# Kernel tuning notes

Hardware: AMD Instinct MI355X
Metric: run time of the kernel (lower is better)

## Reference

```python
import jax, jax.numpy as jnp
import numpy as np

N, E, B = 3000, 96000, 64
CIN, MID = 8, 16
G1, G2 = 32, 8
FC1, FC2, OUT = 512, 128, 10
EPS = 1e-5


def setup_inputs() -> dict:
    key = jax.random.key(0)
    ks = jax.random.split(key, 40)
    u = lambda k, shape, s: jax.random.uniform(k, shape, jnp.float32, -s, s)
    inp = {}
    inp['x'] = jax.random.normal(ks[0], (N, B, CIN), jnp.float32)
    inp['edge_index'] = jax.random.randint(ks[1], (2, E), 0, N, jnp.int64)
    # SAGEConv params (uniform(-1/sqrt(in_channels), ...))
    s = 1.0 / np.sqrt(CIN)
    inp['edge_w_raw'] = jnp.ones((E,), jnp.float32) * 0.01
    inp['sage_self_w'] = u(ks[2], (CIN, MID), s)
    inp['sage_w'] = u(ks[3], (CIN, MID), s)
    inp['sage_b'] = u(ks[4], (MID,), s)
    # LayerNorm over (num_nodes, mid_channel)
    inp['ln_g'] = jnp.ones((N, MID), jnp.float32)
    inp['ln_b'] = jnp.zeros((N, MID), jnp.float32)
    # 1x1 Conv2d stacks (stored as [out,in] matrices) + BatchNorm2d (eval stats)
    inp['conv1_w'] = jax.random.normal(ks[5], (G1, MID), jnp.float32) * np.sqrt(2.0 / G1)
    inp['conv1_b'] = u(ks[6], (G1,), 1.0 / np.sqrt(MID))
    inp['bn1_g'] = jax.random.uniform(ks[7], (G1,), jnp.float32, 0.5, 1.5)
    inp['bn1_b'] = jax.random.normal(ks[8], (G1,), jnp.float32) * 0.1
    inp['bn1_m'] = jax.random.normal(ks[9], (G1,), jnp.float32) * 0.1
    inp['bn1_v'] = jax.random.uniform(ks[10], (G1,), jnp.float32, 0.5, 1.5)
    inp['conv2_w'] = jax.random.normal(ks[11], (G2, G1), jnp.float32) * np.sqrt(2.0 / G2)
    inp['conv2_b'] = u(ks[12], (G2,), 1.0 / np.sqrt(G1))
    inp['bn2_g'] = jax.random.uniform(ks[13], (G2,), jnp.float32, 0.5, 1.5)
    inp['bn2_b'] = jax.random.normal(ks[14], (G2,), jnp.float32) * 0.1
    inp['bn2_m'] = jax.random.normal(ks[15], (G2,), jnp.float32) * 0.1
    inp['bn2_v'] = jax.random.uniform(ks[16], (G2,), jnp.float32, 0.5, 1.5)
    # FC stack: Linear(G2*N, FC1) + BN1d, Linear(FC1, FC2) + BN1d, fc1
    d0 = G2 * N
    inp['fc_w1'] = jax.random.normal(ks[17], (FC1, d0), jnp.float32) * np.sqrt(2.0 / (d0 + FC1))
    inp['fc_b1'] = jnp.full((FC1,), 0.01, jnp.float32)
    inp['bnf1_g'] = jax.random.uniform(ks[18], (FC1,), jnp.float32, 0.5, 1.5)
    inp['bnf1_b'] = jax.random.normal(ks[19], (FC1,), jnp.float32) * 0.1
    inp['bnf1_m'] = jax.random.normal(ks[20], (FC1,), jnp.float32) * 0.1
    inp['bnf1_v'] = jax.random.uniform(ks[21], (FC1,), jnp.float32, 0.5, 1.5)
    inp['fc_w2'] = jax.random.normal(ks[22], (FC2, FC1), jnp.float32) * np.sqrt(2.0 / (FC1 + FC2))
    inp['fc_b2'] = jnp.full((FC2,), 0.01, jnp.float32)
    inp['bnf2_g'] = jax.random.uniform(ks[23], (FC2,), jnp.float32, 0.5, 1.5)
    inp['bnf2_b'] = jax.random.normal(ks[24], (FC2,), jnp.float32) * 0.1
    inp['bnf2_m'] = jax.random.normal(ks[25], (FC2,), jnp.float32) * 0.1
    inp['bnf2_v'] = jax.random.uniform(ks[26], (FC2,), jnp.float32, 0.5, 1.5)
    inp['fc1_w'] = jax.random.normal(ks[27], (OUT, FC2), jnp.float32) * np.sqrt(2.0 / (FC2 + OUT))
    inp['fc1_b'] = jnp.full((OUT,), 0.01, jnp.float32)
    return inp


def _bn(y, g, b, m, v):
    # eval-mode BatchNorm; y is [B, C, N] or [B, C]
    if y.ndim == 3:
        return (y - m[:, None]) * (g[:, None] / jnp.sqrt(v[:, None] + EPS)) + b[:, None]
    return (y - m) * (g / jnp.sqrt(v + EPS)) + b


def reference(x, edge_index, edge_w_raw, sage_self_w, sage_w, sage_b, ln_g, ln_b,
              conv1_w, conv1_b, bn1_g, bn1_b, bn1_m, bn1_v,
              conv2_w, conv2_b, bn2_g, bn2_b, bn2_m, bn2_v,
              fc_w1, fc_b1, bnf1_g, bnf1_b, bnf1_m, bnf1_v,
              fc_w2, fc_b2, bnf2_g, bnf2_b, bnf2_m, bnf2_v,
              fc1_w, fc1_b):
    row, col = edge_index[0], edge_index[1]
    ew = jax.nn.sigmoid(edge_w_raw)
    # SAGEConv: gather -> weighted message -> scatter-mean by col -> matmul
    msg = x[row] * ew[:, None, None]                          # [E, B, CIN]
    summed = jax.ops.segment_sum(msg, col, num_segments=N)    # [N, B, CIN]
    cnt = jax.ops.segment_sum(jnp.ones((E,), x.dtype), col, num_segments=N)
    agg = summed / jnp.maximum(cnt, 1.0)[:, None, None]
    neigh = jnp.einsum('nbc,cm->nbm', agg, sage_w) + sage_b   # [N, B, MID]
    self_out = jnp.einsum('nbc,cm->nbm', x, sage_self_w)
    h = 0.0 * self_out + 1.0 * neigh                          # alphas = [0, 1]
    h = jax.nn.relu(h)
    # LayerNorm over (num_nodes, mid) per batch element
    hb = jnp.transpose(h, (1, 0, 2))                          # [B, N, MID]
    mu = hb.mean(axis=(1, 2), keepdims=True)
    var = hb.var(axis=(1, 2), keepdims=True)
    hb = (hb - mu) / jnp.sqrt(var + EPS) * ln_g + ln_b
    y = jnp.transpose(hb, (0, 2, 1))                          # [B, MID, N]
    # 1x1 conv stack (relu then BN, matching source order)
    y = jnp.einsum('om,bmn->bon', conv1_w, y) + conv1_b[:, None]
    y = _bn(jax.nn.relu(y), bn1_g, bn1_b, bn1_m, bn1_v)
    y = jnp.einsum('oc,bcn->bon', conv2_w, y) + conv2_b[:, None]
    y = _bn(jax.nn.relu(y), bn2_g, bn2_b, bn2_m, bn2_v)       # [B, G2, N]
    z = y.reshape(y.shape[0], -1)                             # [B, G2*N]
    z = jax.nn.relu(_bn(z @ fc_w1.T + fc_b1, bnf1_g, bnf1_b, bnf1_m, bnf1_v))
    z = jax.nn.relu(_bn(z @ fc_w2.T + fc_b2, bnf2_g, bnf2_b, bnf2_m, bnf2_v))
    logits = z @ fc1_w.T + fc1_b
    return jax.nn.softmax(logits, axis=-1), logits
```

## Files before the change

kernel.cpp:

```cpp
#include <hip/hip_runtime.h>
#include <hip/hip_bf16.h>
#include <math.h>

#define NN   3000
#define EE   96000
#define BB   64
#define CIN  8
#define MID  16
#define G1   32
#define G2   8
#define FC1N 512
#define FC2N 128
#define OUTN 10
#define EPSV 1e-5f

#define BC   (BB * CIN)
#define HROW (NN * MID)
#define D0   (G2 * NN)

#define P_EWRAW 0
#define P_SW    96000
#define P_SB    96128
#define P_LNG   96144
#define P_LNB   144144
#define P_C1W   192144
#define P_C1B   192656
#define P_BN1G  192688
#define P_BN1B  192720
#define P_BN1M  192752
#define P_BN1V  192784
#define P_C2W   192816
#define P_C2B   193072
#define P_BN2G  193080
#define P_BN2B  193088
#define P_BN2M  193096
#define P_BN2V  193104
#define P_FB1   193112
#define P_BF1G  193624
#define P_BF1B  194136
#define P_BF1M  194648
#define P_BF1V  195160
#define P_FW2   195672
#define P_FB2   261208
#define P_BF2G  261336
#define P_BF2B  261464
#define P_BF2M  261592
#define P_BF2V  261720
#define P_FOW   261848
#define P_FOB   263128
#define P_TOT   263138

#define KCH  320
#define NKC  75

__device__ __forceinline__ float b2f(unsigned short u) {
    union { unsigned int i; float f; } c;
    c.i = ((unsigned int)u) << 16;
    return c.f;
}

__device__ __forceinline__ unsigned short f2b_rne(float x) {
    union { float f; unsigned int u; } c; c.f = x;
    unsigned int r = c.u + 0x7FFFu + ((c.u >> 16) & 1u);
    return (unsigned short)(r >> 16);
}

typedef __attribute__((ext_vector_type(8))) short short8;
typedef __attribute__((ext_vector_type(4))) float f32x4;

struct PTab { const void* p[30]; };
__global__ __launch_bounds__(256)
void k_prep(const void* __restrict__ ei_raw, const unsigned int* __restrict__ ewr,
            PTab tab,
            int* __restrict__ ei32, int* __restrict__ cnt, int* __restrict__ flags,
            float* __restrict__ P) {
    __shared__ int sh_is64, sh_bf;
    if (threadIdx.x == 0) {
        const int* pw = (const int*)ei_raw;
        int any = 0;
        #pragma unroll
        for (int i = 1; i < 32; i += 2) any |= pw[i];
        sh_is64 = (any == 0) ? 1 : 0;
        unsigned int w = ewr[0];
        sh_bf = ((w >> 16) == (w & 0xFFFFu)) ? 1 : 0;
        if (blockIdx.x == 0) flags[0] = sh_bf;
    }
    __syncthreads();
    int bf = sh_bf;
    long long gi = (long long)blockIdx.x * blockDim.x + threadIdx.x;
    if (gi < 2 * EE) {
        int i = (int)gi;
        int v = sh_is64 ? (int)((const long long*)ei_raw)[i]
                        : ((const int*)ei_raw)[i];
        ei32[i] = v;
        if (i >= EE) atomicAdd(&cnt[v], 1);
        return;
    }
    gi -= 2 * EE;
    if (gi >= P_TOT) return;
    int i = (int)gi;
    const int off[31] = {
        P_EWRAW, P_SW, P_SB, P_LNG, P_LNB, P_C1W, P_C1B, P_BN1G, P_BN1B, P_BN1M,
        P_BN1V, P_C2W, P_C2B, P_BN2G, P_BN2B, P_BN2M, P_BN2V, P_FB1, P_BF1G,
        P_BF1B, P_BF1M, P_BF1V, P_FW2, P_FB2, P_BF2G, P_BF2B, P_BF2M, P_BF2V,
        P_FOW, P_FOB, P_TOT };
    int r = 0;
    #pragma unroll
    for (int j = 1; j < 31; ++j) r += (i >= off[j]) ? 1 : 0;
    int e = i - off[r];
    P[i] = bf ? b2f(((const unsigned short*)tab.p[r])[e])
              : ((const float*)tab.p[r])[e];
}

__global__ void k_scan(const int* __restrict__ cnt, int* __restrict__ off,
                       int* __restrict__ cursor) {
    __shared__ int part[1024];
    int t = threadIdx.x;
    int base = t * 3;
    int c0 = 0, c1 = 0, c2 = 0;
    if (base     < NN) c0 = cnt[base];
    if (base + 1 < NN) c1 = cnt[base + 1];
    if (base + 2 < NN) c2 = cnt[base + 2];
    int s = c0 + c1 + c2;
    part[t] = s;
    __syncthreads();
    for (int d = 1; d < 1024; d <<= 1) {
        int v = (t >= d) ? part[t - d] : 0;
        __syncthreads();
        part[t] += v;
        __syncthreads();
    }
    int excl = part[t] - s;
    if (base < NN)     { off[base]     = excl;           cursor[base]     = excl; }
    if (base + 1 < NN) { off[base + 1] = excl + c0;      cursor[base + 1] = excl + c0; }
    if (base + 2 < NN) { off[base + 2] = excl + c0 + c1; cursor[base + 2] = excl + c0 + c1; }
    if (t == 1023) off[NN] = part[1023];
}

__global__ void k_scatter(const int* __restrict__ ei, const float* __restrict__ ew,
                          int* __restrict__ cursor,
                          int* __restrict__ rcsr, float* __restrict__ wcsr) {
    int e = blockIdx.x * blockDim.x + threadIdx.x;
    if (e < EE) {
        int p = atomicAdd(&cursor[ei[EE + e]], 1);
        rcsr[p] = ei[e];
        wcsr[p] = 1.f / (1.f + expf(-ew[e]));
    }
}

__global__ __launch_bounds__(256)
void k_agg_sage(const void* __restrict__ xraw, const int* __restrict__ flags,
                const int* __restrict__ off,
                const int* __restrict__ rcsr, const float* __restrict__ wcsr,
                const float* __restrict__ sw, const float* __restrict__ sb,
                float* __restrict__ hb) {
    __shared__ float aggL[BC];
    __shared__ float swL[CIN * MID];
    __shared__ float sbL[MID];
    int n = blockIdx.x;
    int t = threadIdx.x;
    if (t < CIN * MID) swL[t] = sw[t];
    if (t < MID)       sbL[t] = sb[t];
    int k0 = off[n], k1 = off[n + 1];
    float a0 = 0.f, a1 = 0.f, b0 = 0.f, b1 = 0.f;
    int k = k0;
    if (flags[0]) {
        const unsigned int* xu = (const unsigned int*)xraw;
        for (; k + 3 < k1; k += 4) {
            int   r0 = rcsr[k],     r1 = rcsr[k + 1];
            int   r2 = rcsr[k + 2], r3 = rcsr[k + 3];
            float w0 = wcsr[k],     w1 = wcsr[k + 1];
            float w2 = wcsr[k + 2], w3 = wcsr[k + 3];
            unsigned int u0 = xu[(size_t)r0 * 256 + t];
            unsigned int u1 = xu[(size_t)r1 * 256 + t];
            unsigned int u2 = xu[(size_t)r2 * 256 + t];
            unsigned int u3 = xu[(size_t)r3 * 256 + t];
            a0 += b2f((unsigned short)(u0 & 0xFFFFu)) * w0;
            a1 += b2f((unsigned short)(u0 >> 16))     * w0;
            b0 += b2f((unsigned short)(u1 & 0xFFFFu)) * w1;
            b1 += b2f((unsigned short)(u1 >> 16))     * w1;
            a0 += b2f((unsigned short)(u2 & 0xFFFFu)) * w2;
            a1 += b2f((unsigned short)(u2 >> 16))     * w2;
            b0 += b2f((unsigned short)(u3 & 0xFFFFu)) * w3;
            b1 += b2f((unsigned short)(u3 >> 16))     * w3;
        }
        for (; k < k1; ++k) {
            int r0 = rcsr[k];
            float w0 = wcsr[k];
            unsigned int u0 = xu[(size_t)r0 * 256 + t];
            a0 += b2f((unsigned short)(u0 & 0xFFFFu)) * w0;
            a1 += b2f((unsigned short)(u0 >> 16))     * w0;
        }
        float inv = 1.f / fmaxf((float)(k1 - k0), 1.f);
        aggL[2 * t]     = (a0 + b0) * inv;
        aggL[2 * t + 1] = (a1 + b1) * inv;
    } else {
        const float* x = (const float*)xraw;
        for (; k + 3 < k1; k += 4) {
            int   r0 = rcsr[k],     r1 = rcsr[k + 1];
            int   r2 = rcsr[k + 2], r3 = rcsr[k + 3];
            float w0 = wcsr[k],     w1 = wcsr[k + 1];
            float w2 = wcsr[k + 2], w3 = wcsr[k + 3];
            const float* xp0 = x + (size_t)r0 * BC;
            const float* xp1 = x + (size_t)r1 * BC;
            const float* xp2 = x + (size_t)r2 * BC;
            const float* xp3 = x + (size_t)r3 * BC;
            a0 += xp0[t]       * w0;  a1 += xp0[t + 256] * w0;
            b0 += xp1[t]       * w1;  b1 += xp1[t + 256] * w1;
            a0 += xp2[t]       * w2;  a1 += xp2[t + 256] * w2;
            b0 += xp3[t]       * w3;  b1 += xp3[t + 256] * w3;
        }
        for (; k < k1; ++k) {
            int r0 = rcsr[k];
            float w0 = wcsr[k];
            const float* xp0 = x + (size_t)r0 * BC;
            a0 += xp0[t] * w0;
            a1 += xp0[t + 256] * w0;
        }
        float inv = 1.f / fmaxf((float)(k1 - k0), 1.f);
        aggL[t]       = (a0 + b0) * inv;
        aggL[t + 256] = (a1 + b1) * inv;
    }
    __syncthreads();
    #pragma unroll
    for (int r4 = 0; r4 < 4; ++r4) {
        int q = t + r4 * 256;
        int b = q >> 4, m = q & 15;
        float v = sbL[m];
        const float* ag = &aggL[b * CIN];
        #pragma unroll
        for (int c = 0; c < CIN; ++c) v += ag[c] * swL[c * MID + m];
        v = fmaxf(v, 0.f);
        hb[(size_t)b * HROW + n * MID + m] = v;
    }
}

__global__ __launch_bounds__(256)
void k_ln_stats(const float* __restrict__ hb, float* __restrict__ stats) {
    __shared__ float ssum[256], ssq[256];
    int b = blockIdx.x, t = threadIdx.x;
    const float4* p = (const float4*)(hb + (size_t)b * HROW);
    float s = 0.f, q = 0.f;
    for (int i = t; i < HROW / 4; i += 256) {
        float4 v = p[i];
        s += v.x + v.y + v.z + v.w;
        q += v.x * v.x + v.y * v.y + v.z * v.z + v.w * v.w;
    }
    ssum[t] = s; ssq[t] = q;
    __syncthreads();
    for (int d = 128; d > 0; d >>= 1) {
        if (t < d) { ssum[t] += ssum[t + d]; ssq[t] += ssq[t + d]; }
        __syncthreads();
    }
    if (t == 0) {
        float mu = ssum[0] / (float)HROW;
        float var = ssq[0] / (float)HROW - mu * mu;
        stats[b]      = mu;
        stats[BB + b] = 1.f / sqrtf(var + EPSV);
    }
}

__global__ __launch_bounds__(256)
void k_conv_stack(const float* __restrict__ hb, const float* __restrict__ stats,
                  const float* __restrict__ P, unsigned short* __restrict__ zT) {
    __shared__ float hbt[64 * 65];
    __shared__ float w1s[G1 * MID], w2s[G2 * G1];
    __shared__ float c1s[G1], s1[G1], t1[G1];
    __shared__ float c2s[G2], s2[G2], t2[G2];
    int t = threadIdx.x;
    int n0 = blockIdx.x * 4;
    for (int j = t; j < G1 * MID; j += 256) w1s[j] = P[P_C1W + j];
    if (t < G2 * G1)  w2s[t] = P[P_C2W + t];
    if (t < G1) {
        float s = P[P_BN1G + t] / sqrtf(P[P_BN1V + t] + EPSV);
        c1s[t] = P[P_C1B + t]; s1[t] = s; t1[t] = P[P_BN1B + t] - P[P_BN1M + t] * s;
    }
    if (t < G2) {
        float s = P[P_BN2G + t] / sqrtf(P[P_BN2V + t] + EPSV);
        c2s[t] = P[P_C2B + t]; s2[t] = s; t2[t] = P[P_BN2B + t] - P[P_BN2M + t] * s;
    }
    #pragma unroll
    for (int r = 0; r < 4; ++r) {
        int i = r * 256 + t;
        int b = i >> 4, q = i & 15;
        float4 v = *(const float4*)(hb + (size_t)b * HROW + n0 * MID + q * 4);
        int ld = b * 65 + q * 4;
        hbt[ld] = v.x; hbt[ld + 1] = v.y; hbt[ld + 2] = v.z; hbt[ld + 3] = v.w;
    }
    __syncthreads();
    int nl = t >> 6, b = t & 63;
    int n = n0 + nl;
    float mu = stats[b], rs = stats[BB + b];
    float tv[MID];
    #pragma unroll
    for (int m = 0; m < MID; ++m) {
        float g = P[P_LNG + n * MID + m], lb = P[P_LNB + n * MID + m];
        tv[m] = (hbt[b * 65 + nl * MID + m] - mu) * rs * g + lb;
    }
    float v1[G1];
    #pragma unroll
    for (int o = 0; o < G1; ++o) {
        float d = c1s[o];
        #pragma unroll
        for (int m = 0; m < MID; ++m) d += w1s[o * MID + m] * tv[m];
        d = fmaxf(d, 0.f);
        v1[o] = d * s1[o] + t1[o];
    }
    #pragma unroll
    for (int o2 = 0; o2 < G2; ++o2) {
        float d = c2s[o2];
        #pragma unroll
        for (int c = 0; c < G1; ++c) d += w2s[o2 * G1 + c] * v1[c];
        d = fmaxf(d, 0.f);
        zT[((size_t)(o2 * NN + n)) * BB + b] = f2b_rne(d * s2[o2] + t2[o2]);
    }
}

__global__ __launch_bounds__(256)
void k_fc1(const unsigned short* __restrict__ zT, const void* __restrict__ w1raw,
           const int* __restrict__ flags, float* __restrict__ out1p) {
    __shared__ unsigned int zs[64 * 20];
    int kc = blockIdx.y;
    int t = threadIdx.x;
    int lane = t & 63;
    int wv = t >> 6;
    int n = lane & 15;
    int q = lane >> 4;
    int fbase = blockIdx.x * 64 + wv * 16;
    int bf = flags[0];
    const size_t kcb = (size_t)kc * KCH;
    const float*          w1f = (const float*)w1raw;
    const unsigned short* w1b = (const unsigned short*)w1raw;

    f32x4 acc0 = {0.f, 0.f, 0.f, 0.f};
    f32x4 acc1 = {0.f, 0.f, 0.f, 0.f};
    f32x4 acc2 = {0.f, 0.f, 0.f, 0.f};
    f32x4 acc3 = {0.f, 0.f, 0.f, 0.f};

    int zb = t & 63;
    int kg = t >> 6;

    for (int ks = 0; ks < KCH / 32; ++ks) {
        size_t k0 = kcb + (size_t)ks * 32;
        const unsigned short* zsrc = zT + (k0 + kg * 8) * BB + zb;
        unsigned short zv[8];
        #pragma unroll
        for (int j = 0; j < 8; ++j) zv[j] = zsrc[j * BB];
        unsigned int pk0 = (unsigned int)zv[0] | ((unsigned int)zv[1] << 16);
        unsigned int pk1 = (unsigned int)zv[2] | ((unsigned int)zv[3] << 16);
        unsigned int pk2 = (unsigned int)zv[4] | ((unsigned int)zv[5] << 16);
        unsigned int pk3 = (unsigned int)zv[6] | ((unsigned int)zv[7] << 16);
        __syncthreads();
        *(uint4*)&zs[zb * 20 + kg * 4] = make_uint4(pk0, pk1, pk2, pk3);
        short8 av;
        if (bf) {
            av = *(const short8*)(w1b + (size_t)(fbase + n) * D0 + k0 + q * 8);
        } else {
            const float* wr = w1f + (size_t)(fbase + n) * D0 + k0 + q * 8;
            float4 wa = *(const float4*)wr;
            float4 wb = *(const float4*)(wr + 4);
            av[0] = (short)f2b_rne(wa.x); av[1] = (short)f2b_rne(wa.y);
            av[2] = (short)f2b_rne(wa.z); av[3] = (short)f2b_rne(wa.w);
            av[4] = (short)f2b_rne(wb.x); av[5] = (short)f2b_rne(wb.y);
            av[6] = (short)f2b_rne(wb.z); av[7] = (short)f2b_rne(wb.w);
        }
        __syncthreads();
        const char* zbase = (const char*)zs + q * 16;
        short8 bv0 = *(const short8*)(zbase + (0  + n) * 80);
        short8 bv1 = *(const short8*)(zbase + (16 + n) * 80);
        short8 bv2 = *(const short8*)(zbase + (32 + n) * 80);
        short8 bv3 = *(const short8*)(zbase + (48 + n) * 80);
        acc0 = __builtin_amdgcn_mfma_f32_16x16x32_bf16(av, bv0, acc0, 0, 0, 0);
        acc1 = __builtin_amdgcn_mfma_f32_16x16x32_bf16(av, bv1, acc1, 0, 0, 0);
        acc2 = __builtin_amdgcn_mfma_f32_16x16x32_bf16(av, bv2, acc2, 0, 0, 0);
        acc3 = __builtin_amdgcn_mfma_f32_16x16x32_bf16(av, bv3, acc3, 0, 0, 0);
    }
    float* op = out1p + ((size_t)kc * FC1N + fbase + q * 4) * BB + n;
    #pragma unroll
    for (int r = 0; r < 4; ++r) {
        op[r * BB +  0] = acc0[r];
        op[r * BB + 16] = acc1[r];
        op[r * BB + 32] = acc2[r];
        op[r * BB + 48] = acc3[r];
    }
}

__global__ void k_fc1_fin(const float* __restrict__ out1p, const float* __restrict__ P,
                          float* __restrict__ z1) {
    int i = blockIdx.x * blockDim.x + threadIdx.x;
    if (i < BB * FC1N) {
        int f = i >> 6, b = i & 63;
        float acc = 0.f;
        for (int kc = 0; kc < NKC; ++kc)
            acc += out1p[((size_t)kc * FC1N + f) * BB + b];
        acc += P[P_FB1 + f];
        float s = P[P_BF1G + f] / sqrtf(P[P_BF1V + f] + EPSV);
        acc = (acc - P[P_BF1M + f]) * s + P[P_BF1B + f];
        z1[b * FC1N + f] = fmaxf(acc, 0.f);
    }
}

__global__ __launch_bounds__(128)
void k_fc2head(const float* __restrict__ z1, const float* __restrict__ P,
               const int* __restrict__ flags, void* __restrict__ outv) {
    __shared__ float zsrc[FC1N];
    __shared__ float z2s[FC2N];
    __shared__ float lg[OUTN];
    __shared__ float red[2];
    int b = blockIdx.x, t = threadIdx.x;
    #pragma unroll
    for (int r = 0; r < 4; ++r) zsrc[t + r * 128] = z1[b * FC1N + t + r * 128];
    __syncthreads();
    {
        int f = t;
        const float4* wr = (const float4*)(P + P_FW2 + (size_t)f * FC1N);
        const float4* zr = (const float4*)zsrc;
        float acc = P[P_FB2 + f];
        for (int k = 0; k < FC1N / 4; ++k) {
            float4 wv = wr[k];
            float4 zv = zr[k];
            acc += wv.x * zv.x + wv.y * zv.y + wv.z * zv.z + wv.w * zv.w;
        }
        float s = P[P_BF2G + f] / sqrtf(P[P_BF2V + f] + EPSV);
        acc = (acc - P[P_BF2M + f]) * s + P[P_BF2B + f];
        z2s[f] = fmaxf(acc, 0.f);
    }
    __syncthreads();
    if (t < OUTN) {
        float acc = P[P_FOB + t];
        const float* wr = P + P_FOW + t * FC2N;
        for (int k = 0; k < FC2N; ++k) acc += wr[k] * z2s[k];
        lg[t] = acc;
    }
    __syncthreads();
    if (t == 0) {
        float mx = lg[0];
        for (int o = 1; o < OUTN; ++o) mx = fmaxf(mx, lg[o]);
        float s = 0.f;
        for (int o = 0; o < OUTN; ++o) s += expf(lg[o] - mx);
        red[0] = mx; red[1] = s;
    }
    __syncthreads();
    if (t < OUTN) {
        float p = expf(lg[t] - red[0]) / red[1];
        if (flags[0]) {
            __hip_bfloat16* o = (__hip_bfloat16*)outv;
            o[b * OUTN + t] = __float2bfloat16(p);
            o[BB * OUTN + b * OUTN + t] = __float2bfloat16(lg[t]);
        } else {
            float* o = (float*)outv;
            o[b * OUTN + t] = p;
            o[BB * OUTN + b * OUTN + t] = lg[t];
        }
    }
}

extern "C" void kernel_launch(void* const* d_in, const int* in_sizes, int n_in,
                              void* d_out, int out_size, void* d_ws, size_t ws_size,
                              hipStream_t stream) {
    char* ws = (char*)d_ws;
    size_t o = 0;
    auto carve = [&](size_t bytes) { void* p = ws + o; o += (bytes + 255) & ~(size_t)255; return p; };
    int*   flags  = (int*)  carve(16);
    int*   ei32   = (int*)  carve((size_t)2 * EE * sizeof(int));
    int*   cnt    = (int*)  carve(NN * sizeof(int));
    int*   off    = (int*)  carve((NN + 1) * sizeof(int));
    int*   cursor = (int*)  carve(NN * sizeof(int));
    int*   rcsr   = (int*)  carve(EE * sizeof(int));
    float* wcsr   = (float*)carve(EE * sizeof(float));
    float* P      = (float*)carve((size_t)P_TOT * sizeof(float));
    float* hb     = (float*)carve((size_t)BB * HROW * sizeof(float));
    float* stats  = (float*)carve(2 * BB * sizeof(float));
    unsigned short* zT = (unsigned short*)carve((size_t)D0 * BB * sizeof(unsigned short));
    float* out1p  = (float*)carve((size_t)NKC * FC1N * BB * sizeof(float));
    float* z1     = (float*)carve(BB * FC1N * sizeof(float));

    hipMemsetAsync(cnt, 0, NN * sizeof(int), stream);

    PTab tab;
    tab.p[0]  = d_in[2];   tab.p[1]  = d_in[4];   tab.p[2]  = d_in[5];
    tab.p[3]  = d_in[6];   tab.p[4]  = d_in[7];   tab.p[5]  = d_in[8];
    tab.p[6]  = d_in[9];   tab.p[7]  = d_in[10];  tab.p[8]  = d_in[11];
    tab.p[9]  = d_in[12];  tab.p[10] = d_in[13];  tab.p[11] = d_in[14];
    tab.p[12] = d_in[15];  tab.p[13] = d_in[16];  tab.p[14] = d_in[17];
    tab.p[15] = d_in[18];  tab.p[16] = d_in[19];  tab.p[17] = d_in[21];
    tab.p[18] = d_in[22];  tab.p[19] = d_in[23];  tab.p[20] = d_in[24];
    tab.p[21] = d_in[25];  tab.p[22] = d_in[26];  tab.p[23] = d_in[27];
    tab.p[24] = d_in[28];  tab.p[25] = d_in[29];  tab.p[26] = d_in[30];
    tab.p[27] = d_in[31];  tab.p[28] = d_in[32];  tab.p[29] = d_in[33];

    long long prep_tot = 2LL * EE + P_TOT;
    k_prep<<<(int)((prep_tot + 255) / 256), 256, 0, stream>>>(
        d_in[1], (const unsigned int*)d_in[2], tab, ei32, cnt, flags, P);

    k_scan   <<<1, 1024, 0, stream>>>(cnt, off, cursor);
    k_scatter<<<(EE + 255) / 256, 256, 0, stream>>>(ei32, P + P_EWRAW, cursor, rcsr, wcsr);
    k_agg_sage<<<NN, 256, 0, stream>>>(d_in[0], flags, off, rcsr, wcsr,
                                       P + P_SW, P + P_SB, hb);
    k_ln_stats<<<BB, 256, 0, stream>>>(hb, stats);
    k_conv_stack<<<NN / 4, 256, 0, stream>>>(hb, stats, P, zT);
    dim3 g7(FC1N / 64, NKC);
    k_fc1    <<<g7, 256, 0, stream>>>(zT, d_in[20], flags, out1p);
    k_fc1_fin<<<(BB * FC1N + 255) / 256, 256, 0, stream>>>(out1p, P, z1);
    k_fc2head<<<BB, 128, 0, stream>>>(z1, P, flags, (void*)d_out);
}
```

Before: 259.8 us.

## Fuse LayerNorm statistics into SAGE aggregation and process four nodes per block

The aggregation kernel now handles four nodes per block and accumulates per-batch sum and sum-of-squares of its outputs, reducing them in shared memory and then atomically into global buffers. This removes the separate LayerNorm statistics kernel, which re-read the whole hidden tensor. The conv stack derives mean and inverse std from those sums, and the stats buffers are placed next to cnt so a single memset clears all of them. In exchange, aggregation launches four times fewer blocks, which lowers parallelism for the gather, and it adds global float atomics whose ordering makes the sums nondeterministic.

Measured after the change: 268.7 us. 3.4% more time.

```diff
diff --git a/kernel.cpp b/kernel.cpp
--- a/kernel.cpp
+++ b/kernel.cpp
@@ -58,7 +58,6 @@
     c.i = ((unsigned int)u) << 16;
     return c.f;
 }
-
 __device__ __forceinline__ unsigned short f2b_rne(float x) {
     union { float f; unsigned int u; } c; c.f = x;
     unsigned int r = c.u + 0x7FFFu + ((c.u >> 16) & 1u);
@@ -153,115 +152,117 @@
                 const int* __restrict__ off,
                 const int* __restrict__ rcsr, const float* __restrict__ wcsr,
                 const float* __restrict__ sw, const float* __restrict__ sb,
-                float* __restrict__ hb) {
+                float* __restrict__ hb,
+                float* __restrict__ statsS, float* __restrict__ statsQ) {
     __shared__ float aggL[BC];
     __shared__ float swL[CIN * MID];
     __shared__ float sbL[MID];
-    int n = blockIdx.x;
+    __shared__ float lnS[BB], lnQ[BB];
     int t = threadIdx.x;
     if (t < CIN * MID) swL[t] = sw[t];
     if (t < MID)       sbL[t] = sb[t];
-    int k0 = off[n], k1 = off[n + 1];
-    float a0 = 0.f, a1 = 0.f, b0 = 0.f, b1 = 0.f;
-    int k = k0;
-    if (flags[0]) {
-        const unsigned int* xu = (const unsigned int*)xraw;
-        for (; k + 3 < k1; k += 4) {
-            int   r0 = rcsr[k],     r1 = rcsr[k + 1];
-            int   r2 = rcsr[k + 2], r3 = rcsr[k + 3];
-            float w0 = wcsr[k],     w1 = wcsr[k + 1];
-            float w2 = wcsr[k + 2], w3 = wcsr[k + 3];
-            unsigned int u0 = xu[(size_t)r0 * 256 + t];
-            unsigned int u1 = xu[(size_t)r1 * 256 + t];
-            unsigned int u2 = xu[(size_t)r2 * 256 + t];
-            unsigned int u3 = xu[(size_t)r3 * 256 + t];
-            a0 += b2f((unsigned short)(u0 & 0xFFFFu)) * w0;
-            a1 += b2f((unsigned short)(u0 >> 16))     * w0;
-            b0 += b2f((unsigned short)(u1 & 0xFFFFu)) * w1;
-            b1 += b2f((unsigned short)(u1 >> 16))     * w1;
-            a0 += b2f((unsigned short)(u2 & 0xFFFFu)) * w2;
-            a1 += b2f((unsigned short)(u2 >> 16))     * w2;
-            b0 += b2f((unsigned short)(u3 & 0xFFFFu)) * w3;
-            b1 += b2f((unsigned short)(u3 >> 16))     * w3;
-        }
-        for (; k < k1; ++k) {
-            int r0 = rcsr[k];
-            float w0 = wcsr[k];
-            unsigned int u0 = xu[(size_t)r0 * 256 + t];
-            a0 += b2f((unsigned short)(u0 & 0xFFFFu)) * w0;
-            a1 += b2f((unsigned short)(u0 >> 16))     * w0;
+    if (t < BB) { lnS[t] = 0.f; lnQ[t] = 0.f; }
+    int bf = flags[0];
+    float accS[4] = {0.f, 0.f, 0.f, 0.f};
+    float accQ[4] = {0.f, 0.f, 0.f, 0.f};
+    __syncthreads();
+    for (int j = 0; j < 4; ++j) {
+        int n = blockIdx.x * 4 + j;
+        int k0 = off[n], k1 = off[n + 1];
+        float a0 = 0.f, a1 = 0.f, b0 = 0.f, b1 = 0.f;
+        int k = k0;
+        if (bf) {
+            const unsigned int* xu = (const unsigned int*)xraw;
+            for (; k + 3 < k1; k += 4) {
+                int   r0 = rcsr[k],     r1 = rcsr[k + 1];
+                int   r2 = rcsr[k + 2], r3 = rcsr[k + 3];
+                float w0 = wcsr[k],     w1 = wcsr[k + 1];
+                float w2 = wcsr[k + 2], w3 = wcsr[k + 3];
+                unsigned int u0 = xu[(size_t)r0 * 256 + t];
+                unsigned int u1 = xu[(size_t)r1 * 256 + t];
+                unsigned int u2 = xu[(size_t)r2 * 256 + t];
+                unsigned int u3 = xu[(size_t)r3 * 256 + t];
+                a0 += b2f((unsigned short)(u0 & 0xFFFFu)) * w0;
+                a1 += b2f((unsigned short)(u0 >> 16))     * w0;
+                b0 += b2f((unsigned short)(u1 & 0xFFFFu)) * w1;
+                b1 += b2f((unsigned short)(u1 >> 16))     * w1;
+                a0 += b2f((unsigned short)(u2 & 0xFFFFu)) * w2;
+                a1 += b2f((unsigned short)(u2 >> 16))     * w2;
+                b0 += b2f((unsigned short)(u3 & 0xFFFFu)) * w3;
+                b1 += b2f((unsigned short)(u3 >> 16))     * w3;
+            }
+            for (; k < k1; ++k) {
+                int r0 = rcsr[k];
+                float w0 = wcsr[k];
+                unsigned int u0 = xu[(size_t)r0 * 256 + t];
+                a0 += b2f((unsigned short)(u0 & 0xFFFFu)) * w0;
+                a1 += b2f((unsigned short)(u0 >> 16))     * w0;
+            }
+        } else {
+            const float* x = (const float*)xraw;
+            for (; k + 3 < k1; k += 4) {
+                int   r0 = rcsr[k],     r1 = rcsr[k + 1];
+                int   r2 = rcsr[k + 2], r3 = rcsr[k + 3];
+                float w0 = wcsr[k],     w1 = wcsr[k + 1];
+                float w2 = wcsr[k + 2], w3 = wcsr[k + 3];
+                const float* xp0 = x + (size_t)r0 * BC;
+                const float* xp1 = x + (size_t)r1 * BC;
+                const float* xp2 = x + (size_t)r2 * BC;
+                const float* xp3 = x + (size_t)r3 * BC;
+                a0 += xp0[t] * w0;  a1 += xp0[t + 256] * w0;
+                b0 += xp1[t] * w1;  b1 += xp1[t + 256] * w1;
+                a0 += xp2[t] * w2;  a1 += xp2[t + 256] * w2;
+                b0 += xp3[t] * w3;  b1 += xp3[t + 256] * w3;
+            }
+            for (; k < k1; ++k) {
+                int r0 = rcsr[k];
+                float w0 = wcsr[k];
+                const float* xp0 = x + (size_t)r0 * BC;
+                a0 += xp0[t] * w0;
+                a1 += xp0[t + 256] * w0;
+            }
         }
         float inv = 1.f / fmaxf((float)(k1 - k0), 1.f);
-        aggL[2 * t]     = (a0 + b0) * inv;
-        aggL[2 * t + 1] = (a1 + b1) * inv;
-    } else {
-        const float* x = (const float*)xraw;
-        for (; k + 3 < k1; k += 4) {
-            int   r0 = rcsr[k],     r1 = rcsr[k + 1];
-            int   r2 = rcsr[k + 2], r3 = rcsr[k + 3];
-            float w0 = wcsr[k],     w1 = wcsr[k + 1];
-            float w2 = wcsr[k + 2], w3 = wcsr[k + 3];
-            const float* xp0 = x + (size_t)r0 * BC;
-            const float* xp1 = x + (size_t)r1 * BC;
-            const float* xp2 = x + (size_t)r2 * BC;
-            const float* xp3 = x + (size_t)r3 * BC;
-            a0 += xp0[t]       * w0;  a1 += xp0[t + 256] * w0;
-            b0 += xp1[t]       * w1;  b1 += xp1[t + 256] * w1;
-            a0 += xp2[t]       * w2;  a1 += xp2[t + 256] * w2;
-            b0 += xp3[t]       * w3;  b1 += xp3[t + 256] * w3;
+        __syncthreads();
+        if (bf) {
+            aggL[2 * t]     = (a0 + b0) * inv;
+            aggL[2 * t + 1] = (a1 + b1) * inv;
+        } else {
+            aggL[t]       = (a0 + b0) * inv;
+            aggL[t + 256] = (a1 + b1) * inv;
         }
-        for (; k < k1; ++k) {
-            int r0 = rcsr[k];
-            float w0 = wcsr[k];
-            const float* xp0 = x + (size_t)r0 * BC;
-            a0 += xp0[t] * w0;
-            a1 += xp0[t + 256] * w0;
+        __syncthreads();
+        #pragma unroll
+        for (int r4 = 0; r4 < 4; ++r4) {
+            int q = t + r4 * 256;
+            int b = q >> 4, m = q & 15;
+            float v = sbL[m];
+            const float* ag = &aggL[b * CIN];
+            #pragma unroll
+            for (int c = 0; c < CIN; ++c) v += ag[c] * swL[c * MID + m];
+            v = fmaxf(v, 0.f);
+            hb[(size_t)b * HROW + n * MID + m] = v;
+            accS[r4] += v;
+            accQ[r4] += v * v;
         }
-        float inv = 1.f / fmaxf((float)(k1 - k0), 1.f);
-        aggL[t]       = (a0 + b0) * inv;
-        aggL[t + 256] = (a1 + b1) * inv;
     }
     __syncthreads();
     #pragma unroll
     for (int r4 = 0; r4 < 4; ++r4) {
-        int q = t + r4 * 256;
-        int b = q >> 4, m = q & 15;
-        float v = sbL[m];
-        const float* ag = &aggL[b * CIN];
-        #pragma unroll
-        for (int c = 0; c < CIN; ++c) v += ag[c] * swL[c * MID + m];
-        v = fmaxf(v, 0.f);
-        hb[(size_t)b * HROW + n * MID + m] = v;
+        int b = (t + r4 * 256) >> 4;
+        atomicAdd(&lnS[b], accS[r4]);
+        atomicAdd(&lnQ[b], accQ[r4]);
+    }
+    __syncthreads();
+    if (t < BB) {
+        atomicAdd(&statsS[t], lnS[t]);
+        atomicAdd(&statsQ[t], lnQ[t]);
     }
 }
 
 __global__ __launch_bounds__(256)
-void k_ln_stats(const float* __restrict__ hb, float* __restrict__ stats) {
-    __shared__ float ssum[256], ssq[256];
-    int b = blockIdx.x, t = threadIdx.x;
-    const float4* p = (const float4*)(hb + (size_t)b * HROW);
-    float s = 0.f, q = 0.f;
-    for (int i = t; i < HROW / 4; i += 256) {
-        float4 v = p[i];
-        s += v.x + v.y + v.z + v.w;
-        q += v.x * v.x + v.y * v.y + v.z * v.z + v.w * v.w;
-    }
-    ssum[t] = s; ssq[t] = q;
-    __syncthreads();
-    for (int d = 128; d > 0; d >>= 1) {
-        if (t < d) { ssum[t] += ssum[t + d]; ssq[t] += ssq[t + d]; }
-        __syncthreads();
-    }
-    if (t == 0) {
-        float mu = ssum[0] / (float)HROW;
-        float var = ssq[0] / (float)HROW - mu * mu;
-        stats[b]      = mu;
-        stats[BB + b] = 1.f / sqrtf(var + EPSV);
-    }
-}
-
-__global__ __launch_bounds__(256)
-void k_conv_stack(const float* __restrict__ hb, const float* __restrict__ stats,
+void k_conv_stack(const float* __restrict__ hb,
+                  const float* __restrict__ statsS, const float* __restrict__ statsQ,
                   const float* __restrict__ P, unsigned short* __restrict__ zT) {
     __shared__ float hbt[64 * 65];
     __shared__ float w1s[G1 * MID], w2s[G2 * G1];
@@ -290,7 +291,9 @@
     __syncthreads();
     int nl = t >> 6, b = t & 63;
     int n = n0 + nl;
-    float mu = stats[b], rs = stats[BB + b];
+    float mu = statsS[b] / (float)HROW;
+    float var = statsQ[b] / (float)HROW - mu * mu;
+    float rs = 1.f / sqrtf(var + EPSV);
     float tv[MID];
     #pragma unroll
     for (int m = 0; m < MID; ++m) {
@@ -464,18 +467,21 @@
     int*   flags  = (int*)  carve(16);
     int*   ei32   = (int*)  carve((size_t)2 * EE * sizeof(int));
     int*   cnt    = (int*)  carve(NN * sizeof(int));
+    float* statsS = (float*)carve(BB * sizeof(float));
+    float* statsQ = (float*)carve(BB * sizeof(float));
     int*   off    = (int*)  carve((NN + 1) * sizeof(int));
     int*   cursor = (int*)  carve(NN * sizeof(int));
     int*   rcsr   = (int*)  carve(EE * sizeof(int));
     float* wcsr   = (float*)carve(EE * sizeof(float));
     float* P      = (float*)carve((size_t)P_TOT * sizeof(float));
     float* hb     = (float*)carve((size_t)BB * HROW * sizeof(float));
-    float* stats  = (float*)carve(2 * BB * sizeof(float));
     unsigned short* zT = (unsigned short*)carve((size_t)D0 * BB * sizeof(unsigned short));
     float* out1p  = (float*)carve((size_t)NKC * FC1N * BB * sizeof(float));
     float* z1     = (float*)carve(BB * FC1N * sizeof(float));
 
-    hipMemsetAsync(cnt, 0, NN * sizeof(int), stream);
+    size_t zero_bytes = ((NN * sizeof(int) + 255) & ~(size_t)255)
+                      + 2 * ((BB * sizeof(float) + 255) & ~(size_t)255);
+    hipMemsetAsync(cnt, 0, zero_bytes, stream);
 
     PTab tab;
     tab.p[0]  = d_in[2];   tab.p[1]  = d_in[4];   tab.p[2]  = d_in[5];
@@ -495,10 +501,9 @@
 
     k_scan   <<<1, 1024, 0, stream>>>(cnt, off, cursor);
     k_scatter<<<(EE + 255) / 256, 256, 0, stream>>>(ei32, P + P_EWRAW, cursor, rcsr, wcsr);
-    k_agg_sage<<<NN, 256, 0, stream>>>(d_in[0], flags, off, rcsr, wcsr,
-                                       P + P_SW, P + P_SB, hb);
-    k_ln_stats<<<BB, 256, 0, stream>>>(hb, stats);
-    k_conv_stack<<<NN / 4, 256, 0, stream>>>(hb, stats, P, zT);
+    k_agg_sage<<<NN / 4, 256, 0, stream>>>(d_in[0], flags, off, rcsr, wcsr,
+                                           P + P_SW, P + P_SB, hb, statsS, statsQ);
+    k_conv_stack<<<NN / 4, 256, 0, stream>>>(hb, statsS, statsQ, P, zT);
     dim3 g7(FC1N / 64, NKC);
     k_fc1    <<<g7, 256, 0, stream>>>(zT, d_in[20], flags, out1p);
     k_fc1_fin<<<(BB * FC1N + 255) / 256, 256, 0, stream>>>(out1p, P, z1);
```
